# Kernel tuning notes

Measured on AMD Instinct MI355X. Metric: run time of the kernel, lower is better.

## Reference

```python
import jax, jax.numpy as jnp
import numpy as np

H = 8
HD = 64
RHO = 0.1


def setup_inputs() -> dict:
    key = jax.random.key(0)
    ks = jax.random.split(key, 5)
    B, L, D = 4, 512, 512
    x = jax.random.normal(ks[0], (B, L, D), dtype=jnp.float32)
    # store projection weights as [in, out] so y = x @ W (equivalent to torch Linear with W.T)
    Wq = jax.random.normal(ks[1], (D, H * HD), dtype=jnp.float32) * 0.02
    Wk = jax.random.normal(ks[2], (D, H * HD), dtype=jnp.float32) * 0.02
    Wv = jax.random.normal(ks[3], (D, H * HD), dtype=jnp.float32) * 0.02
    Wo = jax.random.normal(ks[4], (H * HD, D), dtype=jnp.float32) * 0.02
    return {"x": x, "Wq": Wq, "Wk": Wk, "Wv": Wv, "Wo": Wo}


def _build_adjacency(S):
    # S: [B, H, L, L]. A = (1/L) sum_j [thresholded outer(S[:,:,:,j]) / HD with zero diag]
    B, Hn, L, _ = S.shape
    eye = jnp.eye(L, dtype=bool)
    S_cols = jnp.transpose(S, (3, 0, 1, 2))  # [L, B, H, L]

    def step(acc, s_col):
        # s_col: [B, H, L]; U_j[i,k] = s_col[i] * s_col[k] / HD
        U = s_col[..., :, None] * s_col[..., None, :] / HD  # [B,H,L,L]
        U = jnp.where(eye, 0.0, U)
        A_j = jnp.where(U > RHO, U, 0.0)
        return acc + A_j, None

    A_sum, _ = jax.lax.scan(step, jnp.zeros_like(S), S_cols)
    return A_sum / L


def _normalize_adjacency(A):
    L = A.shape[-1]
    A_tilde = A + jnp.eye(L, dtype=A.dtype)
    D = jnp.clip(A_tilde.sum(axis=-1, keepdims=True), 1e-6, None)
    D_inv_sqrt = D ** -0.5  # [B,H,L,1]
    return D_inv_sqrt * A_tilde * jnp.swapaxes(D_inv_sqrt, -1, -2)


def reference(x, Wq, Wk, Wv, Wo):
    B, L, D = x.shape
    scale = jnp.sqrt(jnp.asarray(HD, dtype=x.dtype))
    def proj(W):
        return jnp.einsum('bld,de->ble', x, W).reshape(B, L, H, HD).transpose(0, 2, 1, 3)
    Q, K, V = proj(Wq), proj(Wk), proj(Wv)  # [B,H,L,HD]
    S = jnp.einsum('bhid,bhjd->bhij', Q, K)  # [B,H,L,L]
    A = _build_adjacency(S)
    A_hat = _normalize_adjacency(A)
    # jump: Phi(S) = A_hat @ S @ A_hat^T
    S_jump = jnp.einsum('bhij,bhjk,bhlk->bhil', A_hat, S, A_hat) / scale
    attn = jax.nn.softmax(S_jump, axis=-1)
    out = jnp.einsum('bhij,bhjd->bhid', attn, V)  # [B,H,L,HD]
    out = out.transpose(0, 2, 1, 3).reshape(B, L, H * HD)
    return jnp.einsum('ble,ed->bld', out, Wo)
```

## Files before the change

### kernel.cpp

```cpp
#include <hip/hip_runtime.h>
#include <math.h>


typedef __attribute__((ext_vector_type(8))) short short8v;
typedef __attribute__((ext_vector_type(4))) float f32x4;

__device__ __forceinline__ void split8(const float* v, unsigned* hi, unsigned* lo)
{
    #pragma unroll
    for (int q = 0; q < 4; ++q) {
        const unsigned b0 = __float_as_uint(v[2 * q])     & 0xFFFF0000u;
        const unsigned b1 = __float_as_uint(v[2 * q + 1]) & 0xFFFF0000u;
        const float d0 = v[2 * q]     - __uint_as_float(b0);
        const float d1 = v[2 * q + 1] - __uint_as_float(b1);
        hi[q] = (b0 >> 16) | b1;
        lo[q] = (__float_as_uint(d0) >> 16) | (__float_as_uint(d1) & 0xFFFF0000u);
    }
}

template<int BT>
__global__ __launch_bounds__(256)
void gemm_mfma(const float* __restrict__ Ap, const float* __restrict__ Bp,
               float* __restrict__ Cp, int K, int lda, int ldb, int ldc,
               long sA, long sB, long sC, float scale)
{
    const float* __restrict__ A = Ap + (long)blockIdx.z * sA;
    const float* __restrict__ B = Bp + (long)blockIdx.z * sB;
    float* __restrict__ C = Cp + (long)blockIdx.z * sC;
    const int m0 = blockIdx.y << 7, n0 = blockIdx.x << 7;

    __shared__ short Ah[128 * 32], Al[128 * 32], Bh[128 * 32], Bl[128 * 32];

    const int tid = threadIdx.x;
    const int lane = tid & 63, wv = tid >> 6;
    const int wr = wv >> 1, wc = wv & 1;

    f32x4 acc[4][4] = {};

    for (int k0 = 0; k0 < K; k0 += 32) {
        {
            const int row = tid >> 1;
            const int swz = (row & 3) ^ ((row >> 2) & 3);
            #pragma unroll
            for (int gg = 0; gg < 2; ++gg) {
                const int g = ((tid & 1) << 1) + gg;
                const float* src = A + (long)(m0 + row) * lda + k0 + (g << 3);
                float v[8];
                *(float4*)&v[0] = *(const float4*)src;
                *(float4*)&v[4] = *(const float4*)(src + 4);
                unsigned hi[4], lo[4];
                split8(v, hi, lo);
                const int off = row * 32 + ((g ^ swz) << 3);
                *(uint4*)&Ah[off] = *(uint4*)hi;
                *(uint4*)&Al[off] = *(uint4*)lo;
            }
        }
        if (BT) {
            const int row = tid >> 1;
            const int swz = (row & 3) ^ ((row >> 2) & 3);
            #pragma unroll
            for (int gg = 0; gg < 2; ++gg) {
                const int g = ((tid & 1) << 1) + gg;
                const float* src = B + (long)(n0 + row) * ldb + k0 + (g << 3);
                float v[8];
                *(float4*)&v[0] = *(const float4*)src;
                *(float4*)&v[4] = *(const float4*)(src + 4);
                unsigned hi[4], lo[4];
                split8(v, hi, lo);
                const int off = row * 32 + ((g ^ swz) << 3);
                *(uint4*)&Bh[off] = *(uint4*)hi;
                *(uint4*)&Bl[off] = *(uint4*)lo;
            }
        } else {
            const int n = tid & 127;
            const int swz = (n & 3) ^ ((n >> 2) & 3);
            #pragma unroll
            for (int gg = 0; gg < 2; ++gg) {
                const int g = ((tid >> 7) << 1) + gg;
                float v[8];
                #pragma unroll
                for (int e = 0; e < 8; ++e)
                    v[e] = B[(long)(k0 + (g << 3) + e) * ldb + n0 + n];
                unsigned hi[4], lo[4];
                split8(v, hi, lo);
                const int off = n * 32 + ((g ^ swz) << 3);
                *(uint4*)&Bh[off] = *(uint4*)hi;
                *(uint4*)&Bl[off] = *(uint4*)lo;
            }
        }
        __syncthreads();

        {
            const int r = lane & 15, g = lane >> 4;
            const int lswz = (r & 3) ^ ((r >> 2) & 3);
            const int gslot = ((g ^ lswz) << 3);
            const int abase = ((wr << 6) + r) * 32 + gslot;
            const int bbase = ((wc << 6) + r) * 32 + gslot;
            short8v afh[4], afl[4], bfh[4], bfl[4];
            #pragma unroll
            for (int f = 0; f < 4; ++f) {
                afh[f] = *(short8v*)&Ah[abase + f * 512];
                afl[f] = *(short8v*)&Al[abase + f * 512];
                bfh[f] = *(short8v*)&Bh[bbase + f * 512];
                bfl[f] = *(short8v*)&Bl[bbase + f * 512];
            }
            #pragma unroll
            for (int fi = 0; fi < 4; ++fi)
                #pragma unroll
                for (int fj = 0; fj < 4; ++fj) {
                    acc[fi][fj] = __builtin_amdgcn_mfma_f32_16x16x32_bf16(
                        afh[fi], bfh[fj], acc[fi][fj], 0, 0, 0);
                    acc[fi][fj] = __builtin_amdgcn_mfma_f32_16x16x32_bf16(
                        afh[fi], bfl[fj], acc[fi][fj], 0, 0, 0);
                    acc[fi][fj] = __builtin_amdgcn_mfma_f32_16x16x32_bf16(
                        afl[fi], bfh[fj], acc[fi][fj], 0, 0, 0);
                }
        }
        __syncthreads();
    }

    const int r = lane & 15, g = lane >> 4;
    #pragma unroll
    for (int fi = 0; fi < 4; ++fi) {
        const int gr0 = m0 + (wr << 6) + fi * 16 + g * 4;
        #pragma unroll
        for (int fj = 0; fj < 4; ++fj) {
            const int gc = n0 + (wc << 6) + fj * 16 + r;
            #pragma unroll
            for (int qq = 0; qq < 4; ++qq)
                C[(long)(gr0 + qq) * ldc + gc] = acc[fi][fj][qq] * scale;
        }
    }
}

__global__ __launch_bounds__(256)
void gemm_qkv_mfma(const float* __restrict__ x, const float* __restrict__ Wq,
                   const float* __restrict__ Wk, const float* __restrict__ Wv,
                   float* __restrict__ QKV)
{
    const int m0 = blockIdx.y << 7;
    const int ng = blockIdx.x << 7;
    const float* __restrict__ W = (ng < 512) ? Wq : (ng < 1024) ? Wk : Wv;
    const int n0 = ng & 511;
    float* __restrict__ C = QKV + (long)(ng >> 9) * (1 << 20);

    __shared__ short Ah[128 * 32], Al[128 * 32], Bh[128 * 32], Bl[128 * 32];

    const int tid = threadIdx.x;
    const int lane = tid & 63, wv = tid >> 6;
    const int wr = wv >> 1, wc = wv & 1;

    f32x4 acc[4][4] = {};

    for (int k0 = 0; k0 < 512; k0 += 32) {
        {
            const int row = tid >> 1;
            const int swz = (row & 3) ^ ((row >> 2) & 3);
            #pragma unroll
            for (int gg = 0; gg < 2; ++gg) {
                const int g = ((tid & 1) << 1) + gg;
                const float* src = x + (long)(m0 + row) * 512 + k0 + (g << 3);
                float v[8];
                *(float4*)&v[0] = *(const float4*)src;
                *(float4*)&v[4] = *(const float4*)(src + 4);
                unsigned hi[4], lo[4];
                split8(v, hi, lo);
                const int off = row * 32 + ((g ^ swz) << 3);
                *(uint4*)&Ah[off] = *(uint4*)hi;
                *(uint4*)&Al[off] = *(uint4*)lo;
            }
        }
        {
            const int n = tid & 127;
            const int swz = (n & 3) ^ ((n >> 2) & 3);
            #pragma unroll
            for (int gg = 0; gg < 2; ++gg) {
                const int g = ((tid >> 7) << 1) + gg;
                float v[8];
                #pragma unroll
                for (int e = 0; e < 8; ++e)
                    v[e] = W[(long)(k0 + (g << 3) + e) * 512 + n0 + n];
                unsigned hi[4], lo[4];
                split8(v, hi, lo);
                const int off = n * 32 + ((g ^ swz) << 3);
                *(uint4*)&Bh[off] = *(uint4*)hi;
                *(uint4*)&Bl[off] = *(uint4*)lo;
            }
        }
        __syncthreads();

        {
            const int r = lane & 15, g = lane >> 4;
            const int lswz = (r & 3) ^ ((r >> 2) & 3);
            const int gslot = ((g ^ lswz) << 3);
            const int abase = ((wr << 6) + r) * 32 + gslot;
            const int bbase = ((wc << 6) + r) * 32 + gslot;
            short8v afh[4], afl[4], bfh[4], bfl[4];
            #pragma unroll
            for (int f = 0; f < 4; ++f) {
                afh[f] = *(short8v*)&Ah[abase + f * 512];
                afl[f] = *(short8v*)&Al[abase + f * 512];
                bfh[f] = *(short8v*)&Bh[bbase + f * 512];
                bfl[f] = *(short8v*)&Bl[bbase + f * 512];
            }
            #pragma unroll
            for (int fi = 0; fi < 4; ++fi)
                #pragma unroll
                for (int fj = 0; fj < 4; ++fj) {
                    acc[fi][fj] = __builtin_amdgcn_mfma_f32_16x16x32_bf16(
                        afh[fi], bfh[fj], acc[fi][fj], 0, 0, 0);
                    acc[fi][fj] = __builtin_amdgcn_mfma_f32_16x16x32_bf16(
                        afh[fi], bfl[fj], acc[fi][fj], 0, 0, 0);
                    acc[fi][fj] = __builtin_amdgcn_mfma_f32_16x16x32_bf16(
                        afl[fi], bfh[fj], acc[fi][fj], 0, 0, 0);
                }
        }
        __syncthreads();
    }

    const int r = lane & 15, g = lane >> 4;
    #pragma unroll
    for (int fi = 0; fi < 4; ++fi) {
        const int gr0 = m0 + (wr << 6) + fi * 16 + g * 4;
        #pragma unroll
        for (int fj = 0; fj < 4; ++fj) {
            const int nl = n0 + (wc << 6) + fj * 16 + r;
            const int h = nl >> 6, d = nl & 63;
            #pragma unroll
            for (int qq = 0; qq < 4; ++qq) {
                const int m = gr0 + qq;
                const int b = m >> 9, l = m & 511;
                C[((long)((b * 8 + h) * 512 + l)) * 64 + d] = acc[fi][fj][qq];
            }
        }
    }
}

__global__ __launch_bounds__(256)
void adj_kernel(const float* __restrict__ S, float* __restrict__ A)
{
    const int bh = blockIdx.y;
    const float* __restrict__ Sh = S + (long)bh * 262144;
    float* __restrict__ Ah = A + (long)bh * 262144;

    int ti = 0, rem = blockIdx.x;
    while (rem >= 8 - ti) { rem -= 8 - ti; ++ti; }
    const int tk = ti + rem;
    const int i0 = ti << 6, k0 = tk << 6;

    __shared__ float smem[8704];

    const int tid  = threadIdx.x;
    const int lane = tid & 63;
    const int wv   = tid >> 6;
    const int ly8  = (lane >> 3) << 3;
    const int lx8  = (lane & 7) << 3;
    const int r4   = lane >> 2;
    const int q    = lane & 3;

    float (*stgL)[68] = (float(*)[68])&smem[wv * 2176];
    float (*stgR)[68] = (float(*)[68])&smem[wv * 2176 + 1088];

    const float RHO64 = 0.1f * 64.0f;

    float acc[8][8] = {};

    const int jw = wv << 7;
    for (int c = 0; c < 8; ++c) {
        const int j0 = jw + (c << 4);
        float4 rl[4], rr[4];
        #pragma unroll
        for (int p = 0; p < 4; ++p) {
            rl[p] = *(const float4*)(Sh + (long)(i0 + r4 + (p << 4)) * 512 + j0 + (q << 2));
            rr[p] = *(const float4*)(Sh + (long)(k0 + r4 + (p << 4)) * 512 + j0 + (q << 2));
        }
        #pragma unroll
        for (int p = 0; p < 4; ++p) {
            const int row = r4 + (p << 4);
            stgL[(q << 2) + 0][row] = rl[p].x;
            stgL[(q << 2) + 1][row] = rl[p].y;
            stgL[(q << 2) + 2][row] = rl[p].z;
            stgL[(q << 2) + 3][row] = rl[p].w;
            stgR[(q << 2) + 0][row] = rr[p].x;
            stgR[(q << 2) + 1][row] = rr[p].y;
            stgR[(q << 2) + 2][row] = rr[p].z;
            stgR[(q << 2) + 3][row] = rr[p].w;
        }
        __builtin_amdgcn_s_waitcnt(0);
        #pragma unroll 4
        for (int jj = 0; jj < 16; ++jj) {
            float a[8], b[8];
            *(float4*)&a[0] = *(const float4*)&stgL[jj][ly8];
            *(float4*)&a[4] = *(const float4*)&stgL[jj][ly8 + 4];
            *(float4*)&b[0] = *(const float4*)&stgR[jj][lx8];
            *(float4*)&b[4] = *(const float4*)&stgR[jj][lx8 + 4];
            #pragma unroll
            for (int i = 0; i < 8; ++i)
                #pragma unroll
                for (int j = 0; j < 8; ++j) {
                    const float u = a[i] * b[j];
                    if (u > RHO64) acc[i][j] += u;
                }
        }
    }

    float* red0 = &smem[0];
    float* red1 = &smem[4352];

    __syncthreads();
    if (wv == 1 || wv == 2) {
        float* dst = (wv == 1 ? red0 : red1) + lane * 68;
        #pragma unroll
        for (int i = 0; i < 8; ++i) {
            *(float4*)(dst + i * 8)     = *(float4*)&acc[i][0];
            *(float4*)(dst + i * 8 + 4) = *(float4*)&acc[i][4];
        }
    }
    __syncthreads();
    if (wv == 0 || wv == 3) {
        const float* src = (wv == 0 ? red0 : red1) + lane * 68;
        #pragma unroll
        for (int i = 0; i < 8; ++i) {
            float4 p0 = *(const float4*)(src + i * 8);
            float4 p1 = *(const float4*)(src + i * 8 + 4);
            acc[i][0] += p0.x; acc[i][1] += p0.y; acc[i][2] += p0.z; acc[i][3] += p0.w;
            acc[i][4] += p1.x; acc[i][5] += p1.y; acc[i][6] += p1.z; acc[i][7] += p1.w;
        }
    }
    __syncthreads();
    if (wv == 3) {
        float* dst = red0 + lane * 68;
        #pragma unroll
        for (int i = 0; i < 8; ++i) {
            *(float4*)(dst + i * 8)     = *(float4*)&acc[i][0];
            *(float4*)(dst + i * 8 + 4) = *(float4*)&acc[i][4];
        }
    }
    __syncthreads();
    if (wv == 0) {
        const float* src = red0 + lane * 68;
        const float SC = 1.0f / 32768.0f;
        float f[8][8];
        #pragma unroll
        for (int i = 0; i < 8; ++i) {
            float4 p0 = *(const float4*)(src + i * 8);
            float4 p1 = *(const float4*)(src + i * 8 + 4);
            f[i][0] = (acc[i][0] + p0.x) * SC;
            f[i][1] = (acc[i][1] + p0.y) * SC;
            f[i][2] = (acc[i][2] + p0.z) * SC;
            f[i][3] = (acc[i][3] + p0.w) * SC;
            f[i][4] = (acc[i][4] + p1.x) * SC;
            f[i][5] = (acc[i][5] + p1.y) * SC;
            f[i][6] = (acc[i][6] + p1.z) * SC;
            f[i][7] = (acc[i][7] + p1.w) * SC;
        }
        if (ti == tk) {
            #pragma unroll
            for (int i = 0; i < 8; ++i)
                #pragma unroll
                for (int j = 0; j < 8; ++j)
                    if (ly8 + i == lx8 + j) f[i][j] = 0.0f;
        }
        #pragma unroll
        for (int i = 0; i < 8; ++i) {
            float* dst = Ah + (long)(i0 + ly8 + i) * 512 + k0 + lx8;
            *(float4*)dst       = make_float4(f[i][0], f[i][1], f[i][2], f[i][3]);
            *(float4*)(dst + 4) = make_float4(f[i][4], f[i][5], f[i][6], f[i][7]);
        }
        if (ti != tk) {
            #pragma unroll
            for (int j = 0; j < 8; ++j) {
                float* dst = Ah + (long)(k0 + lx8 + j) * 512 + i0 + ly8;
                *(float4*)dst       = make_float4(f[0][j], f[1][j], f[2][j], f[3][j]);
                *(float4*)(dst + 4) = make_float4(f[4][j], f[5][j], f[6][j], f[7][j]);
            }
        }
    }
}

__global__ __launch_bounds__(256)
void rowsum_kernel(const float* __restrict__ A, float* __restrict__ R)
{
    const int row = (blockIdx.x << 2) + (threadIdx.x >> 6);
    const int lane = threadIdx.x & 63;
    const float* p = A + (long)row * 512;
    float s = 0.0f;
    #pragma unroll
    for (int t = 0; t < 8; ++t) s += p[lane + (t << 6)];
    #pragma unroll
    for (int off = 32; off; off >>= 1) s += __shfl_xor(s, off, 64);
    if (lane == 0) R[row] = 1.0f / sqrtf(fmaxf(1.0f + s, 1e-6f));
}

__global__ __launch_bounds__(256)
void ahat_kernel(float* __restrict__ A, const float* __restrict__ R)
{
    const long i4 = ((long)blockIdx.x * 256 + threadIdx.x) << 2;
    const long off = i4 & 262143;
    const long bh = i4 >> 18;
    const int i = (int)(off >> 9);
    const int k = (int)(off & 511);
    const float ri = R[(bh << 9) + i];
    const float* Rk = R + (bh << 9) + k;
    float4 v = *(float4*)(A + i4);
    v.x = ri * Rk[0] * (v.x + ((k + 0) == i ? 1.0f : 0.0f));
    v.y = ri * Rk[1] * (v.y + ((k + 1) == i ? 1.0f : 0.0f));
    v.z = ri * Rk[2] * (v.z + ((k + 2) == i ? 1.0f : 0.0f));
    v.w = ri * Rk[3] * (v.w + ((k + 3) == i ? 1.0f : 0.0f));
    *(float4*)(A + i4) = v;
}

__global__ __launch_bounds__(256)
void softmax_kernel(float* __restrict__ P)
{
    float* p = P + (long)blockIdx.x * 512;
    const int t = threadIdx.x;
    float v0 = p[t], v1 = p[t + 256];
    __shared__ float red[256];
    red[t] = fmaxf(v0, v1);
    __syncthreads();
    #pragma unroll
    for (int s = 128; s > 0; s >>= 1) {
        if (t < s) red[t] = fmaxf(red[t], red[t + s]);
        __syncthreads();
    }
    const float mx = red[0];
    __syncthreads();
    const float e0 = __expf(v0 - mx), e1 = __expf(v1 - mx);
    red[t] = e0 + e1;
    __syncthreads();
    #pragma unroll
    for (int s = 128; s > 0; s >>= 1) {
        if (t < s) red[t] += red[t + s];
        __syncthreads();
    }
    const float inv = 1.0f / red[0];
    p[t] = e0 * inv;
    p[t + 256] = e1 * inv;
}

__global__ __launch_bounds__(256)
void gemm_pv(const float* __restrict__ P, const float* __restrict__ V,
             float* __restrict__ O)
{
    const int bh = blockIdx.z;
    const float* Pp = P + (long)bh * 262144;
    const float* Vp = V + (long)bh * 32768;
    float* Op = O + (long)bh * 32768;

    __shared__ float Ps[16][68];
    __shared__ float Vs[16][68];

    const int tid = threadIdx.x;
    const int tx = tid & 15, ty = tid >> 4;
    const int m0 = blockIdx.y << 6;

    float acc[4][4] = {};

    for (int k0 = 0; k0 < 512; k0 += 16) {
        const int r = tid >> 2, c4 = (tid & 3) << 2;
        float4 av = *(const float4*)(Pp + (long)(m0 + r) * 512 + k0 + c4);
        const int rb = tid >> 4, cb = (tid & 15) << 2;
        float4 bv = *(const float4*)(Vp + (long)(k0 + rb) * 64 + cb);

        Ps[c4 + 0][r] = av.x; Ps[c4 + 1][r] = av.y;
        Ps[c4 + 2][r] = av.z; Ps[c4 + 3][r] = av.w;
        *(float4*)&Vs[rb][cb] = bv;
        __syncthreads();

        #pragma unroll
        for (int kk = 0; kk < 16; ++kk) {
            float a[4], b[4];
            *(float4*)a = *(const float4*)&Ps[kk][ty << 2];
            *(float4*)b = *(const float4*)&Vs[kk][tx << 2];
            #pragma unroll
            for (int i = 0; i < 4; ++i)
                #pragma unroll
                for (int j = 0; j < 4; ++j)
                    acc[i][j] = fmaf(a[i], b[j], acc[i][j]);
        }
        __syncthreads();
    }

    #pragma unroll
    for (int i = 0; i < 4; ++i) {
        float4 v = make_float4(acc[i][0], acc[i][1], acc[i][2], acc[i][3]);
        *(float4*)(Op + (long)(m0 + (ty << 2) + i) * 64 + (tx << 2)) = v;
    }
}

__global__ __launch_bounds__(256)
void transO_kernel(const float* __restrict__ O, float* __restrict__ Of)
{
    const long i4 = ((long)blockIdx.x * 256 + threadIdx.x) << 2;
    const int d = (int)(i4 & 63);
    const long rest = i4 >> 6;
    const int l = (int)(rest & 511);
    const long bh = rest >> 9;
    const int h = (int)(bh & 7);
    const long b = bh >> 3;
    const float4 v = *(const float4*)(O + i4);
    *(float4*)(Of + (((b << 9) + l) << 9) + (h << 6) + d) = v;
}

extern "C" void kernel_launch(void* const* d_in, const int* in_sizes, int n_in,
                              void* d_out, int out_size, void* d_ws, size_t ws_size,
                              hipStream_t stream)
{
    const float* x  = (const float*)d_in[0];
    const float* Wq = (const float*)d_in[1];
    const float* Wk = (const float*)d_in[2];
    const float* Wv = (const float*)d_in[3];
    const float* Wo = (const float*)d_in[4];
    float* out = (float*)d_out;

    float* ws = (float*)d_ws;
    float* Q  = ws;
    float* Kt = Q  + (1u << 20);
    float* V  = Kt + (1u << 20);
    float* S  = V  + (1u << 20);
    float* Am = S  + (8u << 20);
    float* T  = Am + (8u << 20);
    float* R  = T  + (8u << 20);
    float* O  = R  + 16384;

    dim3 blk(256);

    gemm_qkv_mfma<<<dim3(12, 16, 1), blk, 0, stream>>>(x, Wq, Wk, Wv, Q);

    gemm_mfma<1><<<dim3(4, 4, 32), blk, 0, stream>>>(Q, Kt, S, 64, 64, 64, 512,
                                                     32768, 32768, 262144, 1.0f);

    adj_kernel<<<dim3(36, 32), blk, 0, stream>>>(S, Am);

    rowsum_kernel<<<dim3(4096), blk, 0, stream>>>(Am, R);

    ahat_kernel<<<dim3(8192), blk, 0, stream>>>(Am, R);

    gemm_mfma<0><<<dim3(4, 4, 32), blk, 0, stream>>>(Am, S, T, 512, 512, 512, 512,
                                                     262144, 262144, 262144, 1.0f);

    gemm_mfma<1><<<dim3(4, 4, 32), blk, 0, stream>>>(T, Am, S, 512, 512, 512, 512,
                                                     262144, 262144, 262144, 0.125f);

    softmax_kernel<<<dim3(16384), blk, 0, stream>>>(S);

    gemm_pv<<<dim3(1, 8, 32), blk, 0, stream>>>(S, V, O);

    transO_kernel<<<dim3(1024), blk, 0, stream>>>(O, Q);

    gemm_mfma<0><<<dim3(4, 16, 1), blk, 0, stream>>>(Q, Wo, out, 512, 512, 512, 512,
                                                     0, 0, 0, 1.0f);
}
```

Baseline: 458.6 us.

## Prefetch adjacency tiles, wave-level softmax, MFMA PV GEMM fused with transpose

The adjacency kernel now double-buffers global loads in registers so the next 16-column chunk is fetched while the current one is computed. Softmax switches from a block-wide shared-memory reduction to one wavefront per row with shuffle reductions. The scalar FP32 PV GEMM is replaced by a split-bf16 (hi/lo, three-product) MFMA GEMM that writes directly into the [B,L,H*HD] layout, removing the separate transpose kernel. The split-bf16 scheme trades some precision against full FP32, and the register prefetch raises register pressure.

After: 498.9 us. +8.8%, slower.

```diff
diff --git a/kernel.cpp b/kernel.cpp
--- a/kernel.cpp
+++ b/kernel.cpp
@@ -264,43 +264,92 @@
     const float RHO64 = 0.1f * 64.0f;
 
     float acc[8][8] = {};
-
     const int jw = wv << 7;
-    for (int c = 0; c < 8; ++c) {
-        const int j0 = jw + (c << 4);
-        float4 rl[4], rr[4];
-        #pragma unroll
-        for (int p = 0; p < 4; ++p) {
-            rl[p] = *(const float4*)(Sh + (long)(i0 + r4 + (p << 4)) * 512 + j0 + (q << 2));
-            rr[p] = *(const float4*)(Sh + (long)(k0 + r4 + (p << 4)) * 512 + j0 + (q << 2));
-        }
-        #pragma unroll
-        for (int p = 0; p < 4; ++p) {
-            const int row = r4 + (p << 4);
-            stgL[(q << 2) + 0][row] = rl[p].x;
-            stgL[(q << 2) + 1][row] = rl[p].y;
-            stgL[(q << 2) + 2][row] = rl[p].z;
-            stgL[(q << 2) + 3][row] = rl[p].w;
-            stgR[(q << 2) + 0][row] = rr[p].x;
-            stgR[(q << 2) + 1][row] = rr[p].y;
-            stgR[(q << 2) + 2][row] = rr[p].z;
-            stgR[(q << 2) + 3][row] = rr[p].w;
-        }
-        __builtin_amdgcn_s_waitcnt(0);
-        #pragma unroll 4
-        for (int jj = 0; jj < 16; ++jj) {
-            float a[8], b[8];
-            *(float4*)&a[0] = *(const float4*)&stgL[jj][ly8];
-            *(float4*)&a[4] = *(const float4*)&stgL[jj][ly8 + 4];
-            *(float4*)&b[0] = *(const float4*)&stgR[jj][lx8];
-            *(float4*)&b[4] = *(const float4*)&stgR[jj][lx8 + 4];
-            #pragma unroll
-            for (int i = 0; i < 8; ++i)
-                #pragma unroll
-                for (int j = 0; j < 8; ++j) {
-                    const float u = a[i] * b[j];
-                    if (u > RHO64) acc[i][j] += u;
+
+    float4 la[4], ra[4], lb[4], rb[4];
+
+    #pragma unroll
+    for (int p = 0; p < 4; ++p) {
+        la[p] = *(const float4*)(Sh + (long)(i0 + r4 + (p << 4)) * 512 + jw + (q << 2));
+        ra[p] = *(const float4*)(Sh + (long)(k0 + r4 + (p << 4)) * 512 + jw + (q << 2));
+    }
+
+    for (int cc = 0; cc < 4; ++cc) {
+        {
+            const int j1 = jw + ((2 * cc + 1) << 4);
+            #pragma unroll
+            for (int p = 0; p < 4; ++p) {
+                lb[p] = *(const float4*)(Sh + (long)(i0 + r4 + (p << 4)) * 512 + j1 + (q << 2));
+                rb[p] = *(const float4*)(Sh + (long)(k0 + r4 + (p << 4)) * 512 + j1 + (q << 2));
+            }
+            #pragma unroll
+            for (int p = 0; p < 4; ++p) {
+                const int row = r4 + (p << 4);
+                stgL[(q << 2) + 0][row] = la[p].x;
+                stgL[(q << 2) + 1][row] = la[p].y;
+                stgL[(q << 2) + 2][row] = la[p].z;
+                stgL[(q << 2) + 3][row] = la[p].w;
+                stgR[(q << 2) + 0][row] = ra[p].x;
+                stgR[(q << 2) + 1][row] = ra[p].y;
+                stgR[(q << 2) + 2][row] = ra[p].z;
+                stgR[(q << 2) + 3][row] = ra[p].w;
+            }
+            asm volatile("s_waitcnt lgkmcnt(0)" ::: "memory");
+            __builtin_amdgcn_sched_barrier(0);
+            #pragma unroll 4
+            for (int jj = 0; jj < 16; ++jj) {
+                float a[8], b[8];
+                *(float4*)&a[0] = *(const float4*)&stgL[jj][ly8];
+                *(float4*)&a[4] = *(const float4*)&stgL[jj][ly8 + 4];
+                *(float4*)&b[0] = *(const float4*)&stgR[jj][lx8];
+                *(float4*)&b[4] = *(const float4*)&stgR[jj][lx8 + 4];
+                #pragma unroll
+                for (int i = 0; i < 8; ++i)
+                    #pragma unroll
+                    for (int j = 0; j < 8; ++j) {
+                        const float u = a[i] * b[j];
+                        if (u > RHO64) acc[i][j] += u;
+                    }
+            }
+        }
+        {
+            if (cc < 3) {
+                const int j2 = jw + ((2 * cc + 2) << 4);
+                #pragma unroll
+                for (int p = 0; p < 4; ++p) {
+                    la[p] = *(const float4*)(Sh + (long)(i0 + r4 + (p << 4)) * 512 + j2 + (q << 2));
+                    ra[p] = *(const float4*)(Sh + (long)(k0 + r4 + (p << 4)) * 512 + j2 + (q << 2));
                 }
+            }
+            #pragma unroll
+            for (int p = 0; p < 4; ++p) {
+                const int row = r4 + (p << 4);
+                stgL[(q << 2) + 0][row] = lb[p].x;
+                stgL[(q << 2) + 1][row] = lb[p].y;
+                stgL[(q << 2) + 2][row] = lb[p].z;
+                stgL[(q << 2) + 3][row] = lb[p].w;
+                stgR[(q << 2) + 0][row] = rb[p].x;
+                stgR[(q << 2) + 1][row] = rb[p].y;
+                stgR[(q << 2) + 2][row] = rb[p].z;
+                stgR[(q << 2) + 3][row] = rb[p].w;
+            }
+            asm volatile("s_waitcnt lgkmcnt(0)" ::: "memory");
+            __builtin_amdgcn_sched_barrier(0);
+            #pragma unroll 4
+            for (int jj = 0; jj < 16; ++jj) {
+                float a[8], b[8];
+                *(float4*)&a[0] = *(const float4*)&stgL[jj][ly8];
+                *(float4*)&a[4] = *(const float4*)&stgL[jj][ly8 + 4];
+                *(float4*)&b[0] = *(const float4*)&stgR[jj][lx8];
+                *(float4*)&b[4] = *(const float4*)&stgR[jj][lx8 + 4];
+                #pragma unroll
+                for (int i = 0; i < 8; ++i)
+                    #pragma unroll
+                    for (int j = 0; j < 8; ++j) {
+                        const float u = a[i] * b[j];
+                        if (u > RHO64) acc[i][j] += u;
+                    }
+            }
         }
     }
 
@@ -413,94 +462,122 @@
 __global__ __launch_bounds__(256)
 void softmax_kernel(float* __restrict__ P)
 {
-    float* p = P + (long)blockIdx.x * 512;
-    const int t = threadIdx.x;
-    float v0 = p[t], v1 = p[t + 256];
-    __shared__ float red[256];
-    red[t] = fmaxf(v0, v1);
-    __syncthreads();
-    #pragma unroll
-    for (int s = 128; s > 0; s >>= 1) {
-        if (t < s) red[t] = fmaxf(red[t], red[t + s]);
+    const int row = (blockIdx.x << 2) + (threadIdx.x >> 6);
+    const int lane = threadIdx.x & 63;
+    float* p = P + (long)row * 512 + (lane << 3);
+    float4 v0 = *(float4*)p;
+    float4 v1 = *(float4*)(p + 4);
+    float mx = fmaxf(fmaxf(fmaxf(v0.x, v0.y), fmaxf(v0.z, v0.w)),
+                     fmaxf(fmaxf(v1.x, v1.y), fmaxf(v1.z, v1.w)));
+    #pragma unroll
+    for (int off = 32; off; off >>= 1) mx = fmaxf(mx, __shfl_xor(mx, off, 64));
+    float e[8];
+    e[0] = __expf(v0.x - mx); e[1] = __expf(v0.y - mx);
+    e[2] = __expf(v0.z - mx); e[3] = __expf(v0.w - mx);
+    e[4] = __expf(v1.x - mx); e[5] = __expf(v1.y - mx);
+    e[6] = __expf(v1.z - mx); e[7] = __expf(v1.w - mx);
+    float s = (((e[0] + e[1]) + (e[2] + e[3])) + ((e[4] + e[5]) + (e[6] + e[7])));
+    #pragma unroll
+    for (int off = 32; off; off >>= 1) s += __shfl_xor(s, off, 64);
+    const float inv = 1.0f / s;
+    *(float4*)p       = make_float4(e[0] * inv, e[1] * inv, e[2] * inv, e[3] * inv);
+    *(float4*)(p + 4) = make_float4(e[4] * inv, e[5] * inv, e[6] * inv, e[7] * inv);
+}
+
+__global__ __launch_bounds__(256)
+void gemm_pv_mfma(const float* __restrict__ P, const float* __restrict__ V,
+                  float* __restrict__ Of)
+{
+    const int bh = blockIdx.z;
+    const float* __restrict__ Pp = P + (long)bh * 262144;
+    const float* __restrict__ Vp = V + (long)bh * 32768;
+    const int bb = bh >> 3, hh = bh & 7;
+    const int m0 = blockIdx.y << 7;
+
+    __shared__ short Ph[128 * 32], Pl[128 * 32], Vh[64 * 32], Vl[64 * 32];
+
+    const int tid = threadIdx.x;
+    const int lane = tid & 63, wv = tid >> 6;
+
+    f32x4 acc[2][4] = {};
+
+    for (int k0 = 0; k0 < 512; k0 += 32) {
+        {
+            const int row = tid >> 1;
+            const int swz = (row & 3) ^ ((row >> 2) & 3);
+            #pragma unroll
+            for (int gg = 0; gg < 2; ++gg) {
+                const int g = ((tid & 1) << 1) + gg;
+                const float* src = Pp + (long)(m0 + row) * 512 + k0 + (g << 3);
+                float v[8];
+                *(float4*)&v[0] = *(const float4*)src;
+                *(float4*)&v[4] = *(const float4*)(src + 4);
+                unsigned hi[4], lo[4];
+                split8(v, hi, lo);
+                const int off = row * 32 + ((g ^ swz) << 3);
+                *(uint4*)&Ph[off] = *(uint4*)hi;
+                *(uint4*)&Pl[off] = *(uint4*)lo;
+            }
+        }
+        {
+            const int n = tid & 63, g = tid >> 6;
+            const int swz = (n & 3) ^ ((n >> 2) & 3);
+            float v[8];
+            #pragma unroll
+            for (int e = 0; e < 8; ++e)
+                v[e] = Vp[(long)(k0 + (g << 3) + e) * 64 + n];
+            unsigned hi[4], lo[4];
+            split8(v, hi, lo);
+            const int off = n * 32 + ((g ^ swz) << 3);
+            *(uint4*)&Vh[off] = *(uint4*)hi;
+            *(uint4*)&Vl[off] = *(uint4*)lo;
+        }
         __syncthreads();
-    }
-    const float mx = red[0];
-    __syncthreads();
-    const float e0 = __expf(v0 - mx), e1 = __expf(v1 - mx);
-    red[t] = e0 + e1;
-    __syncthreads();
-    #pragma unroll
-    for (int s = 128; s > 0; s >>= 1) {
-        if (t < s) red[t] += red[t + s];
+
+        {
+            const int r = lane & 15, g = lane >> 4;
+            const int lswz = (r & 3) ^ ((r >> 2) & 3);
+            const int gslot = ((g ^ lswz) << 3);
+            short8v afh[2], afl[2], bfh[4], bfl[4];
+            #pragma unroll
+            for (int fi = 0; fi < 2; ++fi) {
+                const int abase = ((wv << 5) + (fi << 4) + r) * 32 + gslot;
+                afh[fi] = *(short8v*)&Ph[abase];
+                afl[fi] = *(short8v*)&Pl[abase];
+            }
+            #pragma unroll
+            for (int fj = 0; fj < 4; ++fj) {
+                const int bbase = ((fj << 4) + r) * 32 + gslot;
+                bfh[fj] = *(short8v*)&Vh[bbase];
+                bfl[fj] = *(short8v*)&Vl[bbase];
+            }
+            #pragma unroll
+            for (int fi = 0; fi < 2; ++fi)
+                #pragma unroll
+                for (int fj = 0; fj < 4; ++fj) {
+                    acc[fi][fj] = __builtin_amdgcn_mfma_f32_16x16x32_bf16(
+                        afh[fi], bfh[fj], acc[fi][fj], 0, 0, 0);
+                    acc[fi][fj] = __builtin_amdgcn_mfma_f32_16x16x32_bf16(
+                        afh[fi], bfl[fj], acc[fi][fj], 0, 0, 0);
+                    acc[fi][fj] = __builtin_amdgcn_mfma_f32_16x16x32_bf16(
+                        afl[fi], bfh[fj], acc[fi][fj], 0, 0, 0);
+                }
+        }
         __syncthreads();
     }
-    const float inv = 1.0f / red[0];
-    p[t] = e0 * inv;
-    p[t + 256] = e1 * inv;
-}
-
-__global__ __launch_bounds__(256)
-void gemm_pv(const float* __restrict__ P, const float* __restrict__ V,
-             float* __restrict__ O)
-{
-    const int bh = blockIdx.z;
-    const float* Pp = P + (long)bh * 262144;
-    const float* Vp = V + (long)bh * 32768;
-    float* Op = O + (long)bh * 32768;
-
-    __shared__ float Ps[16][68];
-    __shared__ float Vs[16][68];
-
-    const int tid = threadIdx.x;
-    const int tx = tid & 15, ty = tid >> 4;
-    const int m0 = blockIdx.y << 6;
-
-    float acc[4][4] = {};
-
-    for (int k0 = 0; k0 < 512; k0 += 16) {
-        const int r = tid >> 2, c4 = (tid & 3) << 2;
-        float4 av = *(const float4*)(Pp + (long)(m0 + r) * 512 + k0 + c4);
-        const int rb = tid >> 4, cb = (tid & 15) << 2;
-        float4 bv = *(const float4*)(Vp + (long)(k0 + rb) * 64 + cb);
-
-        Ps[c4 + 0][r] = av.x; Ps[c4 + 1][r] = av.y;
-        Ps[c4 + 2][r] = av.z; Ps[c4 + 3][r] = av.w;
-        *(float4*)&Vs[rb][cb] = bv;
-        __syncthreads();
-
-        #pragma unroll
-        for (int kk = 0; kk < 16; ++kk) {
-            float a[4], b[4];
-            *(float4*)a = *(const float4*)&Ps[kk][ty << 2];
-            *(float4*)b = *(const float4*)&Vs[kk][tx << 2];
-            #pragma unroll
-            for (int i = 0; i < 4; ++i)
-                #pragma unroll
-                for (int j = 0; j < 4; ++j)
-                    acc[i][j] = fmaf(a[i], b[j], acc[i][j]);
-        }
-        __syncthreads();
-    }
-
-    #pragma unroll
-    for (int i = 0; i < 4; ++i) {
-        float4 v = make_float4(acc[i][0], acc[i][1], acc[i][2], acc[i][3]);
-        *(float4*)(Op + (long)(m0 + (ty << 2) + i) * 64 + (tx << 2)) = v;
-    }
-}
-
-__global__ __launch_bounds__(256)
-void transO_kernel(const float* __restrict__ O, float* __restrict__ Of)
-{
-    const long i4 = ((long)blockIdx.x * 256 + threadIdx.x) << 2;
-    const int d = (int)(i4 & 63);
-    const long rest = i4 >> 6;
-    const int l = (int)(rest & 511);
-    const long bh = rest >> 9;
-    const int h = (int)(bh & 7);
-    const long b = bh >> 3;
-    const float4 v = *(const float4*)(O + i4);
-    *(float4*)(Of + (((b << 9) + l) << 9) + (h << 6) + d) = v;
+
+    const int r = lane & 15, g = lane >> 4;
+    #pragma unroll
+    for (int fi = 0; fi < 2; ++fi) {
+        const int l0 = m0 + (wv << 5) + fi * 16 + g * 4;
+        #pragma unroll
+        for (int fj = 0; fj < 4; ++fj) {
+            const int d = fj * 16 + r;
+            #pragma unroll
+            for (int qq = 0; qq < 4; ++qq)
+                Of[((long)((bb << 9) + l0 + qq) << 9) + (hh << 6) + d] = acc[fi][fj][qq];
+        }
+    }
 }
 
 extern "C" void kernel_launch(void* const* d_in, const int* in_sizes, int n_in,
@@ -522,7 +599,6 @@
     float* Am = S  + (8u << 20);
     float* T  = Am + (8u << 20);
     float* R  = T  + (8u << 20);
-    float* O  = R  + 16384;
 
     dim3 blk(256);
 
@@ -543,11 +619,9 @@
     gemm_mfma<1><<<dim3(4, 4, 32), blk, 0, stream>>>(T, Am, S, 512, 512, 512, 512,
                                                      262144, 262144, 262144, 0.125f);
 
-    softmax_kernel<<<dim3(16384), blk, 0, stream>>>(S);
-
-    gemm_pv<<<dim3(1, 8, 32), blk, 0, stream>>>(S, V, O);
-
-    transO_kernel<<<dim3(1024), blk, 0, stream>>>(O, Q);
+    softmax_kernel<<<dim3(4096), blk, 0, stream>>>(S);
+
+    gemm_pv_mfma<<<dim3(1, 4, 32), blk, 0, stream>>>(S, V, Q);
 
     gemm_mfma<0><<<dim3(4, 16, 1), blk, 0, stream>>>(Q, Wo, out, 512, 512, 512, 512,
                                                      0, 0, 0, 1.0f);
```
